# Kernel tuning notes

Measured on AMD Instinct MI355X. Metric: run time of the kernel, lower is better.

Reference implementation:

```python
import jax, jax.numpy as jnp
import numpy as np

S, N, DIN, DH, C, K, E = 12, 50000, 64, 128, 2, 3, 600000
HID = (DH + C) // 2  # 65
LN_EPS = 1e-5


def setup_inputs() -> dict:
    key = jax.random.key(0)
    ks = jax.random.split(key, 16)
    sc = 0.05
    inp = {
        'H': jax.random.normal(ks[0], (S, N, DIN), dtype=jnp.float32),
        'edge_index': jax.random.randint(ks[1], (2, E), 0, N, dtype=jnp.int64),
        # stacked gate params, gate order: 0=i, 1=f, 2=c(cell), 3=o
        'Wx': jax.random.normal(ks[2], (4, K, DIN, DH), dtype=jnp.float32) * sc,
        'bx': jnp.zeros((4, DH), dtype=jnp.float32),
        'Wh': jax.random.normal(ks[3], (4, K, DH, DH), dtype=jnp.float32) * sc,
        'bh': jnp.zeros((4, DH), dtype=jnp.float32),
        'b_gate': jnp.zeros((4, DH), dtype=jnp.float32),
        'wc': jax.random.normal(ks[4], (3, DH), dtype=jnp.float32) * sc,  # peephole: i, f, o
        'ln_gamma': jnp.ones((DH,), dtype=jnp.float32),
        'ln_beta': jnp.zeros((DH,), dtype=jnp.float32),
        'W1': jax.random.normal(ks[5], (DH, HID), dtype=jnp.float32) * sc,
        'b1': jnp.zeros((HID,), dtype=jnp.float32),
        'W2': jax.random.normal(ks[6], (HID, C), dtype=jnp.float32) * sc,
        'b2': jnp.zeros((C,), dtype=jnp.float32),
    }
    return inp


def _cheb_norm(edge_index):
    # sym-normalized, lambda_max=2 => scaled Laplacian Lhat = -D^-1/2 A D^-1/2 (zero diagonal)
    src, dst = edge_index[0], edge_index[1]
    ones = jnp.ones((src.shape[0],), dtype=jnp.float32)
    deg = jax.ops.segment_sum(ones, src, num_segments=N)
    dinv = jnp.where(deg > 0, jax.lax.rsqrt(jnp.maximum(deg, 1.0)), 0.0)
    norm = -dinv[src] * dinv[dst]
    return src, dst, norm


def _cheb_conv(x, W, b, src, dst, norm):
    # x: [N, Din]; W: [K, Din, Dout]. T0=x, T1=Lhat x, Tk=2 Lhat T_{k-1} - T_{k-2}
    Tx0 = x
    out = Tx0 @ W[0]
    if K > 1:
        Tx1 = jax.ops.segment_sum(norm[:, None] * Tx0[src], dst, num_segments=N)
        out = out + Tx1 @ W[1]
        for k in range(2, K):
            Tx2 = 2.0 * jax.ops.segment_sum(norm[:, None] * Tx1[src], dst, num_segments=N) - Tx0
            out = out + Tx2 @ W[k]
            Tx0, Tx1 = Tx1, Tx2
    return out + b


def _decoder(H, edge_index, Wx, bx, Wh, bh, b_gate, wc, ln_gamma, ln_beta, W1, b1, W2, b2):
    src, dst, norm = _cheb_norm(edge_index)

    def step(carry, x_t):
        h, c = carry
        gx = lambda g: _cheb_conv(x_t, Wx[g], bx[g], src, dst, norm)
        gh = lambda g: _cheb_conv(h, Wh[g], bh[g], src, dst, norm)
        i = jax.nn.sigmoid(gx(0) + gh(0) + wc[0] * c + b_gate[0])
        f = jax.nn.sigmoid(gx(1) + gh(1) + wc[1] * c + b_gate[1])
        t = jnp.tanh(gx(2) + gh(2) + b_gate[2])
        c = f * c + i * t
        o = jax.nn.sigmoid(gx(3) + gh(3) + wc[2] * c + b_gate[3])
        h = o * jnp.tanh(c)
        return (h, c), h

    h0 = jnp.zeros((N, DH), dtype=H.dtype)
    (_, _), X = jax.lax.scan(step, (h0, h0), H)  # X: [S, N, DH]

    X = jnp.tanh(X)
    # LayerNorm over conv_dim (last axis here)
    mu = jnp.mean(X, axis=-1, keepdims=True)
    var = jnp.mean(jnp.square(X - mu), axis=-1, keepdims=True)
    X = (X - mu) * jax.lax.rsqrt(var + LN_EPS) * ln_gamma + ln_beta
    # dropout in eval mode: identity
    X = jax.nn.relu(X @ W1 + b1) @ W2 + b2  # [S, N, C]
    X = jax.nn.sigmoid(X)
    return jnp.transpose(X, (1, 2, 0))  # [N, C, S]


def reference(H, edge_index, Wx, bx, Wh, bh, b_gate, wc, ln_gamma, ln_beta, W1, b1, W2, b2):
    return _decoder(H, edge_index, Wx, bx, Wh, bh, b_gate, wc, ln_gamma, ln_beta, W1, b1, W2, b2)
```

## Files before the change

### kernel.cpp

```cpp
#include <hip/hip_runtime.h>
#include <cstdint>
#include <cstddef>

#define S_DIM 12
#define N_NODE 50000
#define N_PAD 50048
#define N_P2 50176
#define D_IN 64
#define D_H 128
#define N_E 600000
#define K_TOT 576
#define N_COL 512
#define HID_P 80
#define N_HID 65
#define AXC 192

#define NB_PREP 1152
#define NB_DEG 2344
#define NB_SPMM 12500
#define NB_LN 782

typedef short bf16x8 __attribute__((ext_vector_type(8)));
typedef float f32x4 __attribute__((ext_vector_type(4)));

__device__ __forceinline__ float bf2f(unsigned short u){
  union { unsigned int i; float f; } v; v.i = ((unsigned int)u) << 16; return v.f;
}
__device__ __forceinline__ unsigned short f2bf(float f){
  union { float f; unsigned int i; } v; v.f = f;
  unsigned int x = v.i;
  return (unsigned short)((x + 0x7fffu + ((x >> 16) & 1u)) >> 16);
}
__device__ __forceinline__ float sigf(float x){ return 1.f/(1.f + __expf(-x)); }
__device__ __forceinline__ float ftanh(float x){
  x = fminf(fmaxf(x, -12.f), 12.f);
  float e = __expf(2.f*x);
  return (e - 1.f)/(e + 1.f);
}
__device__ __forceinline__ void gload16(const void* g, void* lds){
  __builtin_amdgcn_global_load_lds((const __attribute__((address_space(1))) unsigned int*)g,
                                   (__attribute__((address_space(3))) unsigned int*)lds, 16, 0, 0);
}
__device__ __forceinline__ void acc6(float* a, unsigned int p0, unsigned int p1, unsigned int p2, float w){
  unsigned int u[3] = {p0, p1, p2};
#pragma unroll
  for (int i=0;i<3;++i){
    a[2*i]   += w * bf2f((unsigned short)(u[i] & 0xffffu));
    a[2*i+1] += w * bf2f((unsigned short)(u[i] >> 16));
  }
}
__device__ __forceinline__ void acc8(float* a, uint4 h, float w){
  unsigned int u[4] = {h.x, h.y, h.z, h.w};
#pragma unroll
  for (int i=0;i<4;++i){
    a[2*i]   += w * bf2f((unsigned short)(u[i] & 0xffffu));
    a[2*i+1] += w * bf2f((unsigned short)(u[i] >> 16));
  }
}

__global__ void k_setup(const int* __restrict__ ei,
                        const float* __restrict__ Wx, const float* __restrict__ Wh,
                        const float* __restrict__ bx, const float* __restrict__ bh,
                        const float* __restrict__ bg, const float* __restrict__ W1,
                        const float* __restrict__ b1, const float* __restrict__ W2,
                        unsigned short* __restrict__ Bct, float* __restrict__ btot,
                        unsigned short* __restrict__ W1t, float* __restrict__ b1p,
                        float* __restrict__ W2p,
                        int* __restrict__ dsrc, int* __restrict__ ddst)
{
  int bb = blockIdx.x, tid = threadIdx.x;
  if (bb < NB_PREP){
    int idx = bb*256 + tid;
    if (idx < N_COL*K_TOT){
      int cc = idx / K_TOT, k = idx - cc*K_TOT;
      int g = (cc>>4)&3, d = (cc&15) + ((cc>>6)<<4);
      float v;
      if (k < 384){
        int kt = k >> 7, j = k & 127;
        const float* Wg = Wh + (size_t)g*3*128*128;
        if (kt == 0)      v = Wg[(size_t)j*128 + d] - Wg[(size_t)(256+j)*128 + d];
        else if (kt == 1) v = Wg[(size_t)(128+j)*128 + d];
        else              v = 2.f*Wg[(size_t)(256+j)*128 + d];
      } else {
        int kk = k - 384; int kt = kk >> 6, j = kk & 63;
        const float* Wg = Wx + (size_t)g*3*64*128;
        if (kt == 0)      v = Wg[(size_t)j*128 + d] - Wg[(size_t)(128+j)*128 + d];
        else if (kt == 1) v = Wg[(size_t)(64+j)*128 + d];
        else              v = 2.f*Wg[(size_t)(128+j)*128 + d];
      }
      Bct[(size_t)cc*K_TOT + k] = f2bf(v);
    }
    if (idx < N_COL) btot[idx] = bx[idx] + bh[idx] + bg[idx];
    if (idx < HID_P*D_H){ int c = idx >> 7, k = idx & 127;
      W1t[idx] = (c < N_HID) ? f2bf(W1[k*N_HID + c]) : (unsigned short)0; }
    if (idx < HID_P) b1p[idx] = (idx < N_HID) ? b1[idx] : 0.f;
    if (idx < HID_P*2){ int c = idx >> 1, j = idx & 1; W2p[idx] = (c < N_HID) ? W2[c*2 + j] : 0.f; }
  } else {
    int e = (bb - NB_PREP)*256 + tid;
    if (e < N_E){
      atomicAdd(&dsrc[ei[e]], 1);
      atomicAdd(&ddst[ei[N_E + e]], 1);
    }
  }
}

#define XP_STR 2056
__global__ __launch_bounds__(256,3) void k_xprep(const float* __restrict__ H,
                        unsigned short* __restrict__ Xtr, unsigned short* __restrict__ Axt)
{
  __shared__ unsigned short xls[12*XP_STR];
  int bb = blockIdx.x, tid = threadIdx.x;
  int n0 = bb*32;
  int nn = tid >> 3;
  int d  = (tid & 7)*8;
  int gn = n0 + nn;
#pragma unroll
  for (int t=0;t<12;++t){
    unsigned short u[8];
    if (gn < N_NODE){
      const float* hp = H + ((size_t)t*N_NODE + gn)*64 + d;
      float4 a = *(const float4*)hp;
      float4 b = *(const float4*)(hp+4);
      u[0]=f2bf(a.x); u[1]=f2bf(a.y); u[2]=f2bf(a.z); u[3]=f2bf(a.w);
      u[4]=f2bf(b.x); u[5]=f2bf(b.y); u[6]=f2bf(b.z); u[7]=f2bf(b.w);
    } else {
#pragma unroll
      for (int i=0;i<8;++i) u[i]=0;
    }
    *(int4*)(xls + t*XP_STR + nn*64 + d) = *(const int4*)u;
    *(int4*)(Axt + ((size_t)t*N_PAD + gn)*AXC + d) = *(const int4*)u;
    if (gn >= N_NODE){
      *(int4*)(Axt + ((size_t)t*N_PAD + gn)*AXC + 64 + d)  = *(const int4*)u;
      *(int4*)(Axt + ((size_t)t*N_PAD + gn)*AXC + 128 + d) = *(const int4*)u;
    }
  }
  __syncthreads();
#pragma unroll
  for (int rep=0; rep<8; ++rep){
    int cIdx = rep*256 + tid;
    int n = cIdx >> 6, dd = cIdx & 63;
    unsigned int w0[3], w1[3];
#pragma unroll
    for (int i=0;i<3;++i){
      unsigned short a0 = xls[(2*i  )*XP_STR + n*64 + dd];
      unsigned short a1 = xls[(2*i+1)*XP_STR + n*64 + dd];
      unsigned short b0 = xls[(6+2*i)*XP_STR + n*64 + dd];
      unsigned short b1 = xls[(7+2*i)*XP_STR + n*64 + dd];
      w0[i] = (unsigned int)a0 | ((unsigned int)a1<<16);
      w1[i] = (unsigned int)b0 | ((unsigned int)b1<<16);
    }
    size_t cell = ((size_t)(n0+n)*64 + dd)*6;
    unsigned int* p0 = (unsigned int*)(Xtr + cell);
    unsigned int* p1 = (unsigned int*)(Xtr + (size_t)N_PAD*384 + cell);
    p0[0]=w0[0]; p0[1]=w0[1]; p0[2]=w0[2];
    p1[0]=w1[0]; p1[1]=w1[1]; p1[2]=w1[2];
  }
}

__global__ void k_scan1d(const int* __restrict__ in, int* __restrict__ outp, int* __restrict__ part,
                         const int* __restrict__ dsrc, float* __restrict__ dinv){
  __shared__ int sm[256];
  int tid = threadIdx.x;
  int i = blockIdx.x*256 + tid;
  dinv[i] = (dsrc[i] > 0) ? rsqrtf((float)dsrc[i]) : 0.f;
  int v = in[i];
  int x = v;
  sm[tid] = x; __syncthreads();
  for (int off=1; off<256; off<<=1){
    int y = (tid >= off) ? sm[tid-off] : 0;
    __syncthreads();
    x += y; sm[tid] = x; __syncthreads();
  }
  outp[i] = x - v;
  if (tid == 255) part[blockIdx.x] = x;
}
__global__ void k_scan3f(const int* __restrict__ outp, const int* __restrict__ part,
                         int* __restrict__ offs){
  __shared__ int sm[256];
  int tid = threadIdx.x;
  int v = (tid < N_P2/256) ? part[tid] : 0;
  int x = v; sm[tid] = x; __syncthreads();
  for (int off=1; off<256; off<<=1){
    int y = (tid >= off) ? sm[tid-off] : 0;
    __syncthreads();
    x += y; sm[tid] = x; __syncthreads();
  }
  int pref = (blockIdx.x > 0) ? sm[blockIdx.x - 1] : 0;
  int i = blockIdx.x*256 + tid;
  offs[i] = outp[i] + pref;
}
__global__ void k_csr(const int* __restrict__ ei, const float* __restrict__ dinv,
                      const int* __restrict__ offs, int* __restrict__ cursor,
                      int2* __restrict__ cedge){
  int e = blockIdx.x*256 + threadIdx.x;
  if (e < N_E){
    int s = ei[e], d = ei[N_E + e];
    int pos = atomicAdd(&cursor[d], 1);
    float w = -dinv[s]*dinv[d];
    cedge[offs[d] + pos] = make_int2(s, __float_as_int(w));
  }
}

__global__ void k_xspmm1(const unsigned short* __restrict__ Xtr, unsigned short* __restrict__ Axt,
                         unsigned short* __restrict__ U1tr,
                         const int* __restrict__ offs, const int2* __restrict__ cedge){
  int bb = blockIdx.x;
  int h = (bb >= NB_SPMM) ? 1 : 0;
  const unsigned short* Xh = Xtr + (size_t)h*N_PAD*384;
  unsigned short* AxtH = Axt + (size_t)h*6*N_PAD*AXC;
  unsigned short* Uh = U1tr + (size_t)h*N_PAD*384;
  int n = (bb - h*NB_SPMM)*4 + (threadIdx.x >> 6);
  int l = threadIdx.x & 63;
  if (n >= N_NODE) return;
  int beg = offs[n], end = offs[n+1];
  int ce = end - 1;
  float a[6];
#pragma unroll
  for (int t=0;t<6;++t) a[t] = 0.f;
  for (int q = beg; q < end; q += 6){
    int2 e0 = cedge[min(q,   ce)];
    int2 e1 = cedge[min(q+1, ce)];
    int2 e2 = cedge[min(q+2, ce)];
    int2 e3 = cedge[min(q+3, ce)];
    int2 e4 = cedge[min(q+4, ce)];
    int2 e5 = cedge[min(q+5, ce)];
    float w0 = __int_as_float(e0.y);
    float w1 = (q+1 < end) ? __int_as_float(e1.y) : 0.f;
    float w2 = (q+2 < end) ? __int_as_float(e2.y) : 0.f;
    float w3 = (q+3 < end) ? __int_as_float(e3.y) : 0.f;
    float w4 = (q+4 < end) ? __int_as_float(e4.y) : 0.f;
    float w5 = (q+5 < end) ? __int_as_float(e5.y) : 0.f;
    const unsigned int* r0 = (const unsigned int*)(Xh + ((size_t)e0.x*64 + l)*6);
    const unsigned int* r1 = (const unsigned int*)(Xh + ((size_t)e1.x*64 + l)*6);
    const unsigned int* r2 = (const unsigned int*)(Xh + ((size_t)e2.x*64 + l)*6);
    const unsigned int* r3 = (const unsigned int*)(Xh + ((size_t)e3.x*64 + l)*6);
    const unsigned int* r4 = (const unsigned int*)(Xh + ((size_t)e4.x*64 + l)*6);
    const unsigned int* r5 = (const unsigned int*)(Xh + ((size_t)e5.x*64 + l)*6);
    unsigned int p00=r0[0], p01=r0[1], p02=r0[2];
    unsigned int p10=r1[0], p11=r1[1], p12=r1[2];
    unsigned int p20=r2[0], p21=r2[1], p22=r2[2];
    unsigned int p30=r3[0], p31=r3[1], p32=r3[2];
    unsigned int p40=r4[0], p41=r4[1], p42=r4[2];
    unsigned int p50=r5[0], p51=r5[1], p52=r5[2];
    acc6(a, p00, p01, p02, w0);
    acc6(a, p10, p11, p12, w1);
    acc6(a, p20, p21, p22, w2);
    acc6(a, p30, p31, p32, w3);
    acc6(a, p40, p41, p42, w4);
    acc6(a, p50, p51, p52, w5);
  }
  unsigned short u[6];
#pragma unroll
  for (int t=0;t<6;++t){
    u[t] = f2bf(a[t]);
    AxtH[((size_t)t*N_PAD + n)*AXC + 64 + l] = u[t];
  }
  unsigned int* op = (unsigned int*)(Uh + ((size_t)n*64 + l)*6);
#pragma unroll
  for (int i=0;i<3;++i) op[i] = (unsigned int)u[2*i] | ((unsigned int)u[2*i+1] << 16);
}
__global__ void k_xspmm2(const unsigned short* __restrict__ U1tr, unsigned short* __restrict__ Axt,
                         const int* __restrict__ offs, const int2* __restrict__ cedge){
  int bb = blockIdx.x;
  int h = (bb >= NB_SPMM) ? 1 : 0;
  const unsigned short* Uh = U1tr + (size_t)h*N_PAD*384;
  unsigned short* AxtH = Axt + (size_t)h*6*N_PAD*AXC;
  int n = (bb - h*NB_SPMM)*4 + (threadIdx.x >> 6);
  int l = threadIdx.x & 63;
  if (n >= N_NODE) return;
  int beg = offs[n], end = offs[n+1];
  int ce = end - 1;
  float a[6];
#pragma unroll
  for (int t=0;t<6;++t) a[t] = 0.f;
  for (int q = beg; q < end; q += 6){
    int2 e0 = cedge[min(q,   ce)];
    int2 e1 = cedge[min(q+1, ce)];
    int2 e2 = cedge[min(q+2, ce)];
    int2 e3 = cedge[min(q+3, ce)];
    int2 e4 = cedge[min(q+4, ce)];
    int2 e5 = cedge[min(q+5, ce)];
    float w0 = __int_as_float(e0.y);
    float w1 = (q+1 < end) ? __int_as_float(e1.y) : 0.f;
    float w2 = (q+2 < end) ? __int_as_float(e2.y) : 0.f;
    float w3 = (q+3 < end) ? __int_as_float(e3.y) : 0.f;
    float w4 = (q+4 < end) ? __int_as_float(e4.y) : 0.f;
    float w5 = (q+5 < end) ? __int_as_float(e5.y) : 0.f;
    const unsigned int* r0 = (const unsigned int*)(Uh + ((size_t)e0.x*64 + l)*6);
    const unsigned int* r1 = (const unsigned int*)(Uh + ((size_t)e1.x*64 + l)*6);
    const unsigned int* r2 = (const unsigned int*)(Uh + ((size_t)e2.x*64 + l)*6);
    const unsigned int* r3 = (const unsigned int*)(Uh + ((size_t)e3.x*64 + l)*6);
    const unsigned int* r4 = (const unsigned int*)(Uh + ((size_t)e4.x*64 + l)*6);
    const unsigned int* r5 = (const unsigned int*)(Uh + ((size_t)e5.x*64 + l)*6);
    unsigned int p00=r0[0], p01=r0[1], p02=r0[2];
    unsigned int p10=r1[0], p11=r1[1], p12=r1[2];
    unsigned int p20=r2[0], p21=r2[1], p22=r2[2];
    unsigned int p30=r3[0], p31=r3[1], p32=r3[2];
    unsigned int p40=r4[0], p41=r4[1], p42=r4[2];
    unsigned int p50=r5[0], p51=r5[1], p52=r5[2];
    acc6(a, p00, p01, p02, w0);
    acc6(a, p10, p11, p12, w1);
    acc6(a, p20, p21, p22, w2);
    acc6(a, p30, p31, p32, w3);
    acc6(a, p40, p41, p42, w4);
    acc6(a, p50, p51, p52, w5);
  }
#pragma unroll
  for (int t=0;t<6;++t)
    AxtH[((size_t)t*N_PAD + n)*AXC + 128 + l] = f2bf(a[t]);
}

__device__ __forceinline__ void spmm1_body(int n, int l,
    const unsigned short* __restrict__ Hc, unsigned short* __restrict__ U,
    const int* __restrict__ offs, const int2* __restrict__ cedge)
{
  if (n >= N_NODE) return;
  int sub = l >> 4, fl = l & 15;
  int beg = offs[n], end = offs[n+1];
  int ce = end - 1;
  float a[8];
#pragma unroll
  for (int j=0;j<8;++j) a[j] = 0.f;
  for (int q = beg; q < end; q += 16){
    int i0 = q + sub, i1 = q + 4 + sub, i2 = q + 8 + sub, i3 = q + 12 + sub;
    int2 e0 = cedge[min(i0, ce)];
    int2 e1 = cedge[min(i1, ce)];
    int2 e2 = cedge[min(i2, ce)];
    int2 e3 = cedge[min(i3, ce)];
    float w0 = (i0 < end) ? __int_as_float(e0.y) : 0.f;
    float w1 = (i1 < end) ? __int_as_float(e1.y) : 0.f;
    float w2 = (i2 < end) ? __int_as_float(e2.y) : 0.f;
    float w3 = (i3 < end) ? __int_as_float(e3.y) : 0.f;
    uint4 h0 = *(const uint4*)(Hc + (size_t)e0.x*128 + fl*8);
    uint4 h1 = *(const uint4*)(Hc + (size_t)e1.x*128 + fl*8);
    uint4 h2 = *(const uint4*)(Hc + (size_t)e2.x*128 + fl*8);
    uint4 h3 = *(const uint4*)(Hc + (size_t)e3.x*128 + fl*8);
    acc8(a, h0, w0);
    acc8(a, h1, w1);
    acc8(a, h2, w2);
    acc8(a, h3, w3);
  }
#pragma unroll
  for (int j=0;j<8;++j){
    a[j] += __shfl_xor(a[j], 16);
    a[j] += __shfl_xor(a[j], 32);
  }
  if (sub == 0){
    unsigned short o[8];
#pragma unroll
    for (int j=0;j<8;++j) o[j] = f2bf(a[j]);
    *(uint4*)(U + (size_t)n*256 + fl*8) = *(const uint4*)o;
  }
}

__global__ void k_spmm2(unsigned short* __restrict__ U,
                        const int* __restrict__ offs, const int2* __restrict__ cedge){
  int n = blockIdx.x*4 + (threadIdx.x >> 6);
  int l = threadIdx.x & 63;
  if (n >= N_NODE) return;
  int sub = l >> 4, fl = l & 15;
  int beg = offs[n], end = offs[n+1];
  int ce = end - 1;
  float a[8];
#pragma unroll
  for (int j=0;j<8;++j) a[j] = 0.f;
  for (int q = beg; q < end; q += 16){
    int i0 = q + sub, i1 = q + 4 + sub, i2 = q + 8 + sub, i3 = q + 12 + sub;
    int2 e0 = cedge[min(i0, ce)];
    int2 e1 = cedge[min(i1, ce)];
    int2 e2 = cedge[min(i2, ce)];
    int2 e3 = cedge[min(i3, ce)];
    float w0 = (i0 < end) ? __int_as_float(e0.y) : 0.f;
    float w1 = (i1 < end) ? __int_as_float(e1.y) : 0.f;
    float w2 = (i2 < end) ? __int_as_float(e2.y) : 0.f;
    float w3 = (i3 < end) ? __int_as_float(e3.y) : 0.f;
    uint4 h0 = *(const uint4*)(U + (size_t)e0.x*256 + fl*8);
    uint4 h1 = *(const uint4*)(U + (size_t)e1.x*256 + fl*8);
    uint4 h2 = *(const uint4*)(U + (size_t)e2.x*256 + fl*8);
    uint4 h3 = *(const uint4*)(U + (size_t)e3.x*256 + fl*8);
    acc8(a, h0, w0);
    acc8(a, h1, w1);
    acc8(a, h2, w2);
    acc8(a, h3, w3);
  }
#pragma unroll
  for (int j=0;j<8;++j){
    a[j] += __shfl_xor(a[j], 16);
    a[j] += __shfl_xor(a[j], 32);
  }
  if (sub == 0){
    unsigned short o[8];
#pragma unroll
    for (int j=0;j<8;++j) o[j] = f2bf(a[j]);
    *(uint4*)(U + (size_t)n*256 + 128 + fl*8) = *(const uint4*)o;
  }
}

__device__ __forceinline__ void lnmlp_body(int n0,
    const unsigned short* __restrict__ Hn,
    const unsigned short* __restrict__ W1t, const float* __restrict__ b1p,
    const float* __restrict__ W2p, const float* __restrict__ b2,
    const float* __restrict__ gam, const float* __restrict__ bet,
    float* __restrict__ out, int t)
{
  __shared__ __align__(16) unsigned short xn[64*128];
  __shared__ __align__(16) unsigned short w1s[HID_P*128];
  __shared__ float w2s[HID_P*2];
  __shared__ float b1s[HID_P];
  __shared__ float b2s[2];
  int tid = threadIdx.x;
  for (int i = tid; i < HID_P*128/8; i += 256) ((int4*)w1s)[i] = ((const int4*)W1t)[i];
  if (tid < HID_P*2) w2s[tid] = W2p[tid];
  if (tid < HID_P)   b1s[tid] = b1p[tid];
  if (tid < 2)       b2s[tid] = b2[tid];
  int row = tid >> 2, part = tid & 3;
  int n = n0 + row;
  float vals[32];
  float s = 0.f, ss = 0.f;
  if (n < N_NODE){
    const unsigned short* hp = Hn + (size_t)n*128 + part*32;
#pragma unroll
    for (int k=0;k<32;++k){
      float x = ftanh(bf2f(hp[k]));
      vals[k] = x; s += x; ss += x*x;
    }
  } else {
#pragma unroll
    for (int k=0;k<32;++k) vals[k] = 0.f;
  }
  s  += __shfl_xor(s,1);  s  += __shfl_xor(s,2);
  ss += __shfl_xor(ss,1); ss += __shfl_xor(ss,2);
  float mu = s * (1.f/128.f);
  float var = ss * (1.f/128.f) - mu*mu;
  float inv = rsqrtf(fmaxf(var, 0.f) + 1e-5f);
#pragma unroll
  for (int k=0;k<32;++k){
    int d = part*32 + k;
    xn[row*128 + d] = f2bf((vals[k]-mu)*inv*gam[d] + bet[d]);
  }
  __syncthreads();
  int w = tid >> 6, l = tid & 63;
  const f32x4 vzero = {0.f,0.f,0.f,0.f};
  f32x4 acc[5];
#pragma unroll
  for (int tj=0;tj<5;++tj) acc[tj] = vzero;
#pragma unroll
  for (int kk=0;kk<4;++kk){
    bf16x8 a = *(const bf16x8*)(xn + (w*16 + (l&15))*128 + kk*32 + (l>>4)*8);
#pragma unroll
    for (int tj=0;tj<5;++tj){
      bf16x8 b = *(const bf16x8*)(w1s + (tj*16 + (l&15))*128 + kk*32 + (l>>4)*8);
      acc[tj] = __builtin_amdgcn_mfma_f32_16x16x32_bf16(a, b, acc[tj], 0,0,0);
    }
  }
#pragma unroll
  for (int r=0;r<4;++r){
    int rn = n0 + w*16 + (l>>4)*4 + r;
    float p0 = 0.f, p1 = 0.f;
#pragma unroll
    for (int tj=0;tj<5;++tj){
      int col = tj*16 + (l&15);
      float hv = fmaxf(acc[tj][r] + b1s[col], 0.f);
      p0 += hv * w2s[col*2];
      p1 += hv * w2s[col*2+1];
    }
    p0 += __shfl_xor(p0,1); p0 += __shfl_xor(p0,2); p0 += __shfl_xor(p0,4); p0 += __shfl_xor(p0,8);
    p1 += __shfl_xor(p1,1); p1 += __shfl_xor(p1,2); p1 += __shfl_xor(p1,4); p1 += __shfl_xor(p1,8);
    if ((l & 15) == 0 && rn < N_NODE){
      float* op = out + (size_t)rn*24 + t;
      op[0]  = sigf(p0 + b2s[0]);
      op[12] = sigf(p1 + b2s[1]);
    }
  }
}

__global__ void k_sp1ln(const unsigned short* __restrict__ Hc, unsigned short* __restrict__ U,
                        const int* __restrict__ offs, const int2* __restrict__ cedge,
                        const unsigned short* __restrict__ W1t, const float* __restrict__ b1p,
                        const float* __restrict__ W2p, const float* __restrict__ b2,
                        const float* __restrict__ gam, const float* __restrict__ bet,
                        float* __restrict__ out, int tprev)
{
  int bb = blockIdx.x;
  if (bb < NB_LN){
    lnmlp_body(bb*64, Hc, W1t, b1p, W2p, b2, gam, bet, out, tprev);
  } else {
    spmm1_body((bb - NB_LN)*4 + (threadIdx.x >> 6), threadIdx.x & 63, Hc, U, offs, cedge);
  }
}

__global__ __launch_bounds__(256,2) void k_lnmlp(const unsigned short* __restrict__ Hn,
                        const unsigned short* __restrict__ W1t, const float* __restrict__ b1p,
                        const float* __restrict__ W2p, const float* __restrict__ b2,
                        const float* __restrict__ gam, const float* __restrict__ bet,
                        float* __restrict__ out, int t)
{
  lnmlp_body(blockIdx.x*64, Hn, W1t, b1p, W2p, b2, gam, bet, out, t);
}

__global__ __launch_bounds__(256,3) void k_gemm(
    const unsigned short* __restrict__ Hc, const unsigned short* __restrict__ U,
    const unsigned short* __restrict__ Axt,
    const unsigned short* __restrict__ Bct, const float* __restrict__ btot,
    const float* __restrict__ wc, unsigned short* __restrict__ cst,
    unsigned short* __restrict__ Hn, int it0)
{
  int L = blockIdx.y*4 + blockIdx.x;
  int xcd = L & 7, li = L >> 3;
  int by = xcd + ((li >> 2) << 3);
  int bx = li & 3;
  if (by >= N_PAD/128) return;
  __shared__ __align__(16) unsigned short As[128*64];
  __shared__ __align__(16) unsigned short Bs[128*64];
  int tid = threadIdx.x;
  int w = tid >> 6, l = tid & 63;
  int n0 = bx * 128;
  int m0 = by * 128;
  int wr = w >> 1, wn = w & 1;
  int dd = (((bx<<1) + wn) << 4) | (l & 15);
  float cof[4][4];
#pragma unroll
  for (int i=0;i<4;++i)
#pragma unroll
    for (int r=0;r<4;++r){
      int row = m0 + wr*64 + i*16 + (l>>4)*4 + r;
      cof[i][r] = bf2f(cst[(size_t)row*128 + dd]);
    }
  float b_i = btot[dd], b_f = btot[128+dd], b_t = btot[256+dd], b_o = btot[384+dd];
  float wci = wc[dd], wcf = wc[128+dd], wco = wc[256+dd];
  const f32x4 vzero = {0.f,0.f,0.f,0.f};
  f32x4 acc[4][4];
#pragma unroll
  for (int i=0;i<4;++i)
#pragma unroll
    for (int j=0;j<4;++j) acc[i][j] = vzero;
  for (int it=it0; it<9; ++it){
    const unsigned short* Ab; int astr, acol;
    if (it < 2)      { Ab = Hc;  astr = 128; acol = it*64; }
    else if (it < 6) { Ab = U;   astr = 256; acol = (it-2)*64; }
    else             { Ab = Axt; astr = AXC; acol = (it-6)*64; }
    if (it != it0) __syncthreads();
#pragma unroll
    for (int i=0;i<4;++i){
      int rr = w*32 + i*8;
      int row = rr + (l>>3);
      gload16(Ab  + (size_t)(m0+row)*astr + acol + (l&7)*8, (void*)(As + rr*64));
      gload16(Bct + (size_t)(n0+row)*K_TOT + it*64 + (l&7)*8, (void*)(Bs + rr*64));
    }
    __syncthreads();
#pragma unroll
    for (int kk=0; kk<2; ++kk){
      bf16x8 af[4], bfv[4];
#pragma unroll
      for (int i=0;i<4;++i) af[i]  = *(const bf16x8*)(As + (wr*64 + i*16 + (l&15))*64 + kk*32 + (l>>4)*8);
#pragma unroll
      for (int j=0;j<4;++j) bfv[j] = *(const bf16x8*)(Bs + (wn*64 + j*16 + (l&15))*64 + kk*32 + (l>>4)*8);
#pragma unroll
      for (int i=0;i<4;++i)
#pragma unroll
        for (int j=0;j<4;++j)
          acc[i][j] = __builtin_amdgcn_mfma_f32_16x16x32_bf16(af[i], bfv[j], acc[i][j], 0,0,0);
    }
  }
#pragma unroll
  for (int i=0;i<4;++i){
    int row0 = m0 + wr*64 + i*16 + (l>>4)*4;
#pragma unroll
    for (int r=0;r<4;++r){
      int row = row0 + r;
      float co = cof[i][r];
      float gi = sigf(acc[i][0][r] + b_i + wci*co);
      float gf = sigf(acc[i][1][r] + b_f + wcf*co);
      float tt = ftanh(acc[i][2][r] + b_t);
      float cn = gf*co + gi*tt;
      float go = sigf(acc[i][3][r] + b_o + wco*cn);
      float h = go * ftanh(cn);
      cst[(size_t)row*128 + dd] = f2bf(cn);
      Hn[(size_t)row*128 + dd] = f2bf(h);
    }
  }
}

extern "C" void kernel_launch(void* const* d_in, const int* in_sizes, int n_in,
                              void* d_out, int out_size, void* d_ws, size_t ws_size,
                              hipStream_t stream)
{
  const float* H   = (const float*)d_in[0];
  const int*   ei  = (const int*)d_in[1];
  const float* Wx  = (const float*)d_in[2];
  const float* bx  = (const float*)d_in[3];
  const float* Wh  = (const float*)d_in[4];
  const float* bh  = (const float*)d_in[5];
  const float* bg  = (const float*)d_in[6];
  const float* wc  = (const float*)d_in[7];
  const float* gam = (const float*)d_in[8];
  const float* bet = (const float*)d_in[9];
  const float* W1  = (const float*)d_in[10];
  const float* b1  = (const float*)d_in[11];
  const float* W2  = (const float*)d_in[12];
  const float* b2  = (const float*)d_in[13];
  float* out = (float*)d_out;
  (void)in_sizes; (void)n_in; (void)out_size; (void)ws_size;

  char* p = (char*)d_ws;
  auto alloc = [&](size_t bytes)->char*{ char* r = p; p += (bytes + 255) & ~(size_t)255; return r; };
  char* zbase = p;
  unsigned short* c_st = (unsigned short*)alloc((size_t)N_PAD*128*2);
  int* dsrc   = (int*)alloc((size_t)N_P2*4);
  int* ddst   = (int*)alloc((size_t)N_P2*4);
  int* cursor = (int*)alloc((size_t)N_P2*4);
  size_t zbytes = (size_t)(p - zbase);
  unsigned short* Hbuf0 = (unsigned short*)alloc((size_t)N_PAD*128*2);
  unsigned short* Hbuf1 = (unsigned short*)alloc((size_t)N_PAD*128*2);
  unsigned short* Ubuf  = (unsigned short*)alloc((size_t)N_PAD*256*2);
  unsigned short* Xtr   = (unsigned short*)alloc((size_t)N_PAD*768*2);
  unsigned short* U1tr  = (unsigned short*)alloc((size_t)N_PAD*768*2);
  unsigned short* Axt   = (unsigned short*)alloc((size_t)S_DIM*N_PAD*AXC*2);
  unsigned short* Bct   = (unsigned short*)alloc((size_t)N_COL*K_TOT*2);
  float*          btot  = (float*)alloc(N_COL*4);
  unsigned short* W1t   = (unsigned short*)alloc(HID_P*128*2);
  float*          b1p   = (float*)alloc(HID_P*4);
  float*          W2p   = (float*)alloc(HID_P*2*4);
  float*          dinv  = (float*)alloc((size_t)N_P2*4);
  int*            offs  = (int*)alloc((size_t)(N_P2+256)*4);
  int*            outp  = (int*)alloc((size_t)N_P2*4);
  int*            partb = (int*)alloc(256*4);
  int2*           cedge = (int2*)alloc((size_t)N_E*8);

  hipMemsetAsync(zbase, 0, zbytes, stream);
  k_setup<<<NB_PREP + NB_DEG, 256, 0, stream>>>(ei, Wx, Wh, bx, bh, bg,
      W1, b1, W2, Bct, btot, W1t, b1p, W2p, dsrc, ddst);
  k_xprep<<<N_PAD/32, 256, 0, stream>>>(H, Xtr, Axt);
  k_scan1d<<<N_P2/256, 256, 0, stream>>>(ddst, outp, partb, dsrc, dinv);
  k_scan3f<<<N_P2/256, 256, 0, stream>>>(outp, partb, offs);
  k_csr<<<NB_DEG, 256, 0, stream>>>(ei, dinv, offs, cursor, cedge);
  k_xspmm1<<<2*NB_SPMM, 256, 0, stream>>>(Xtr, Axt, U1tr, offs, cedge);
  k_xspmm2<<<2*NB_SPMM, 256, 0, stream>>>(U1tr, Axt, offs, cedge);

  k_gemm<<<dim3(4, 392), 256, 0, stream>>>(Hbuf0, Ubuf, Axt,
      Bct, btot, wc, c_st, Hbuf1, 6);
  for (int t = 1; t < S_DIM; ++t){
    unsigned short* Hc = (t & 1) ? Hbuf1 : Hbuf0;
    unsigned short* Hn = (t & 1) ? Hbuf0 : Hbuf1;
    k_sp1ln<<<NB_SPMM + NB_LN, 256, 0, stream>>>(Hc, Ubuf, offs, cedge,
        W1t, b1p, W2p, b2, gam, bet, out, t-1);
    k_spmm2<<<NB_SPMM, 256, 0, stream>>>(Ubuf, offs, cedge);
    k_gemm<<<dim3(4, 392), 256, 0, stream>>>(Hc, Ubuf,
        Axt + (size_t)t*N_PAD*AXC, Bct, btot, wc, c_st, Hn, 0);
  }
  k_lnmlp<<<NB_LN, 256, 0, stream>>>(Hbuf0, W1t, b1p, W2p, b2, gam, bet, out, 11);
}
```

Before: 1.905 ms.

## Split input-side Chebyshev SpMM and overlap most of it with timestep 1

Before the recurrence, only the input Chebyshev propagation columns needed for timesteps 0 and 1 are computed. The remaining input columns are computed as extra blocks folded into the timestep-1 spmm1/LN and spmm2 launches. This reorders k_sp1ln so spmm blocks come first, and in the GEMM it defers the cell-state and bias loads until after the MFMA loop to lower register pressure. The aim is to fill idle GPU capacity in the small recurrent kernels and shorten the serial prologue, at the cost of a larger, more divergent fused launch at t=1.

```diff
diff --git a/kernel.cpp b/kernel.cpp
--- a/kernel.cpp
+++ b/kernel.cpp
@@ -19,6 +19,7 @@
 #define NB_DEG 2344
 #define NB_SPMM 12500
 #define NB_LN 782
+#define NB_X 25000
 
 typedef short bf16x8 __attribute__((ext_vector_type(8)));
 typedef float f32x4 __attribute__((ext_vector_type(4)));
@@ -40,14 +41,6 @@
 __device__ __forceinline__ void gload16(const void* g, void* lds){
   __builtin_amdgcn_global_load_lds((const __attribute__((address_space(1))) unsigned int*)g,
                                    (__attribute__((address_space(3))) unsigned int*)lds, 16, 0, 0);
-}
-__device__ __forceinline__ void acc6(float* a, unsigned int p0, unsigned int p1, unsigned int p2, float w){
-  unsigned int u[3] = {p0, p1, p2};
-#pragma unroll
-  for (int i=0;i<3;++i){
-    a[2*i]   += w * bf2f((unsigned short)(u[i] & 0xffffu));
-    a[2*i+1] += w * bf2f((unsigned short)(u[i] >> 16));
-  }
 }
 __device__ __forceinline__ void acc8(float* a, uint4 h, float w){
   unsigned int u[4] = {h.x, h.y, h.z, h.w};
@@ -201,113 +194,102 @@
   }
 }
 
-__global__ void k_xspmm1(const unsigned short* __restrict__ Xtr, unsigned short* __restrict__ Axt,
-                         unsigned short* __restrict__ U1tr,
-                         const int* __restrict__ offs, const int2* __restrict__ cedge){
-  int bb = blockIdx.x;
-  int h = (bb >= NB_SPMM) ? 1 : 0;
-  const unsigned short* Xh = Xtr + (size_t)h*N_PAD*384;
-  unsigned short* AxtH = Axt + (size_t)h*6*N_PAD*AXC;
-  unsigned short* Uh = U1tr + (size_t)h*N_PAD*384;
-  int n = (bb - h*NB_SPMM)*4 + (threadIdx.x >> 6);
+template<int D0, int ND>
+__device__ __forceinline__ void xsp1_body(const unsigned short* __restrict__ Xh,
+    unsigned short* __restrict__ AxtH, unsigned short* __restrict__ Uh,
+    int n, int l, const int* __restrict__ offs, const int2* __restrict__ cedge)
+{
+  int beg = offs[n], end = offs[n+1];
+  int ce = end - 1;
+  float a[2*ND];
+#pragma unroll
+  for (int i=0;i<2*ND;++i) a[i] = 0.f;
+  for (int q = beg; q < end; q += 6){
+    int2 e[6]; float w[6];
+#pragma unroll
+    for (int j=0;j<6;++j){
+      e[j] = cedge[min(q+j, ce)];
+      w[j] = (q+j < end) ? __int_as_float(e[j].y) : 0.f;
+    }
+    unsigned int p[6][ND];
+#pragma unroll
+    for (int j=0;j<6;++j){
+      const unsigned int* r = (const unsigned int*)(Xh + ((size_t)e[j].x*64 + l)*6);
+#pragma unroll
+      for (int i=0;i<ND;++i) p[j][i] = r[D0+i];
+    }
+#pragma unroll
+    for (int j=0;j<6;++j)
+#pragma unroll
+      for (int i=0;i<ND;++i){
+        a[2*i]   += w[j]*bf2f((unsigned short)(p[j][i] & 0xffffu));
+        a[2*i+1] += w[j]*bf2f((unsigned short)(p[j][i] >> 16));
+      }
+  }
+  unsigned int* uc = (unsigned int*)(Uh + ((size_t)n*64 + l)*6);
+#pragma unroll
+  for (int i=0;i<ND;++i){
+    unsigned short u0 = f2bf(a[2*i]), u1 = f2bf(a[2*i+1]);
+    int tp = 2*(D0+i);
+    AxtH[((size_t)tp*N_PAD + n)*AXC + 64 + l]     = u0;
+    AxtH[((size_t)(tp+1)*N_PAD + n)*AXC + 64 + l] = u1;
+    uc[D0+i] = (unsigned int)u0 | ((unsigned int)u1 << 16);
+  }
+}
+template<int D0, int ND>
+__device__ __forceinline__ void xsp2_body(const unsigned short* __restrict__ Uh,
+    unsigned short* __restrict__ AxtH,
+    int n, int l, const int* __restrict__ offs, const int2* __restrict__ cedge)
+{
+  int beg = offs[n], end = offs[n+1];
+  int ce = end - 1;
+  float a[2*ND];
+#pragma unroll
+  for (int i=0;i<2*ND;++i) a[i] = 0.f;
+  for (int q = beg; q < end; q += 6){
+    int2 e[6]; float w[6];
+#pragma unroll
+    for (int j=0;j<6;++j){
+      e[j] = cedge[min(q+j, ce)];
+      w[j] = (q+j < end) ? __int_as_float(e[j].y) : 0.f;
+    }
+    unsigned int p[6][ND];
+#pragma unroll
+    for (int j=0;j<6;++j){
+      const unsigned int* r = (const unsigned int*)(Uh + ((size_t)e[j].x*64 + l)*6);
+#pragma unroll
+      for (int i=0;i<ND;++i) p[j][i] = r[D0+i];
+    }
+#pragma unroll
+    for (int j=0;j<6;++j)
+#pragma unroll
+      for (int i=0;i<ND;++i){
+        a[2*i]   += w[j]*bf2f((unsigned short)(p[j][i] & 0xffffu));
+        a[2*i+1] += w[j]*bf2f((unsigned short)(p[j][i] >> 16));
+      }
+  }
+#pragma unroll
+  for (int i=0;i<ND;++i){
+    int tp = 2*(D0+i);
+    AxtH[((size_t)tp*N_PAD + n)*AXC + 128 + l]     = f2bf(a[2*i]);
+    AxtH[((size_t)(tp+1)*N_PAD + n)*AXC + 128 + l] = f2bf(a[2*i+1]);
+  }
+}
+
+__global__ void k_xsp1_t01(const unsigned short* __restrict__ Xtr, unsigned short* __restrict__ Axt,
+                           unsigned short* __restrict__ U1tr,
+                           const int* __restrict__ offs, const int2* __restrict__ cedge){
+  int n = blockIdx.x*4 + (threadIdx.x >> 6);
   int l = threadIdx.x & 63;
   if (n >= N_NODE) return;
-  int beg = offs[n], end = offs[n+1];
-  int ce = end - 1;
-  float a[6];
-#pragma unroll
-  for (int t=0;t<6;++t) a[t] = 0.f;
-  for (int q = beg; q < end; q += 6){
-    int2 e0 = cedge[min(q,   ce)];
-    int2 e1 = cedge[min(q+1, ce)];
-    int2 e2 = cedge[min(q+2, ce)];
-    int2 e3 = cedge[min(q+3, ce)];
-    int2 e4 = cedge[min(q+4, ce)];
-    int2 e5 = cedge[min(q+5, ce)];
-    float w0 = __int_as_float(e0.y);
-    float w1 = (q+1 < end) ? __int_as_float(e1.y) : 0.f;
-    float w2 = (q+2 < end) ? __int_as_float(e2.y) : 0.f;
-    float w3 = (q+3 < end) ? __int_as_float(e3.y) : 0.f;
-    float w4 = (q+4 < end) ? __int_as_float(e4.y) : 0.f;
-    float w5 = (q+5 < end) ? __int_as_float(e5.y) : 0.f;
-    const unsigned int* r0 = (const unsigned int*)(Xh + ((size_t)e0.x*64 + l)*6);
-    const unsigned int* r1 = (const unsigned int*)(Xh + ((size_t)e1.x*64 + l)*6);
-    const unsigned int* r2 = (const unsigned int*)(Xh + ((size_t)e2.x*64 + l)*6);
-    const unsigned int* r3 = (const unsigned int*)(Xh + ((size_t)e3.x*64 + l)*6);
-    const unsigned int* r4 = (const unsigned int*)(Xh + ((size_t)e4.x*64 + l)*6);
-    const unsigned int* r5 = (const unsigned int*)(Xh + ((size_t)e5.x*64 + l)*6);
-    unsigned int p00=r0[0], p01=r0[1], p02=r0[2];
-    unsigned int p10=r1[0], p11=r1[1], p12=r1[2];
-    unsigned int p20=r2[0], p21=r2[1], p22=r2[2];
-    unsigned int p30=r3[0], p31=r3[1], p32=r3[2];
-    unsigned int p40=r4[0], p41=r4[1], p42=r4[2];
-    unsigned int p50=r5[0], p51=r5[1], p52=r5[2];
-    acc6(a, p00, p01, p02, w0);
-    acc6(a, p10, p11, p12, w1);
-    acc6(a, p20, p21, p22, w2);
-    acc6(a, p30, p31, p32, w3);
-    acc6(a, p40, p41, p42, w4);
-    acc6(a, p50, p51, p52, w5);
-  }
-  unsigned short u[6];
-#pragma unroll
-  for (int t=0;t<6;++t){
-    u[t] = f2bf(a[t]);
-    AxtH[((size_t)t*N_PAD + n)*AXC + 64 + l] = u[t];
-  }
-  unsigned int* op = (unsigned int*)(Uh + ((size_t)n*64 + l)*6);
-#pragma unroll
-  for (int i=0;i<3;++i) op[i] = (unsigned int)u[2*i] | ((unsigned int)u[2*i+1] << 16);
-}
-__global__ void k_xspmm2(const unsigned short* __restrict__ U1tr, unsigned short* __restrict__ Axt,
-                         const int* __restrict__ offs, const int2* __restrict__ cedge){
-  int bb = blockIdx.x;
-  int h = (bb >= NB_SPMM) ? 1 : 0;
-  const unsigned short* Uh = U1tr + (size_t)h*N_PAD*384;
-  unsigned short* AxtH = Axt + (size_t)h*6*N_PAD*AXC;
-  int n = (bb - h*NB_SPMM)*4 + (threadIdx.x >> 6);
+  xsp1_body<0,1>(Xtr, Axt, U1tr, n, l, offs, cedge);
+}
+__global__ void k_xsp2_t01(const unsigned short* __restrict__ U1tr, unsigned short* __restrict__ Axt,
+                           const int* __restrict__ offs, const int2* __restrict__ cedge){
+  int n = blockIdx.x*4 + (threadIdx.x >> 6);
   int l = threadIdx.x & 63;
   if (n >= N_NODE) return;
-  int beg = offs[n], end = offs[n+1];
-  int ce = end - 1;
-  float a[6];
-#pragma unroll
-  for (int t=0;t<6;++t) a[t] = 0.f;
-  for (int q = beg; q < end; q += 6){
-    int2 e0 = cedge[min(q,   ce)];
-    int2 e1 = cedge[min(q+1, ce)];
-    int2 e2 = cedge[min(q+2, ce)];
-    int2 e3 = cedge[min(q+3, ce)];
-    int2 e4 = cedge[min(q+4, ce)];
-    int2 e5 = cedge[min(q+5, ce)];
-    float w0 = __int_as_float(e0.y);
-    float w1 = (q+1 < end) ? __int_as_float(e1.y) : 0.f;
-    float w2 = (q+2 < end) ? __int_as_float(e2.y) : 0.f;
-    float w3 = (q+3 < end) ? __int_as_float(e3.y) : 0.f;
-    float w4 = (q+4 < end) ? __int_as_float(e4.y) : 0.f;
-    float w5 = (q+5 < end) ? __int_as_float(e5.y) : 0.f;
-    const unsigned int* r0 = (const unsigned int*)(Uh + ((size_t)e0.x*64 + l)*6);
-    const unsigned int* r1 = (const unsigned int*)(Uh + ((size_t)e1.x*64 + l)*6);
-    const unsigned int* r2 = (const unsigned int*)(Uh + ((size_t)e2.x*64 + l)*6);
-    const unsigned int* r3 = (const unsigned int*)(Uh + ((size_t)e3.x*64 + l)*6);
-    const unsigned int* r4 = (const unsigned int*)(Uh + ((size_t)e4.x*64 + l)*6);
-    const unsigned int* r5 = (const unsigned int*)(Uh + ((size_t)e5.x*64 + l)*6);
-    unsigned int p00=r0[0], p01=r0[1], p02=r0[2];
-    unsigned int p10=r1[0], p11=r1[1], p12=r1[2];
-    unsigned int p20=r2[0], p21=r2[1], p22=r2[2];
-    unsigned int p30=r3[0], p31=r3[1], p32=r3[2];
-    unsigned int p40=r4[0], p41=r4[1], p42=r4[2];
-    unsigned int p50=r5[0], p51=r5[1], p52=r5[2];
-    acc6(a, p00, p01, p02, w0);
-    acc6(a, p10, p11, p12, w1);
-    acc6(a, p20, p21, p22, w2);
-    acc6(a, p30, p31, p32, w3);
-    acc6(a, p40, p41, p42, w4);
-    acc6(a, p50, p51, p52, w5);
-  }
-#pragma unroll
-  for (int t=0;t<6;++t)
-    AxtH[((size_t)t*N_PAD + n)*AXC + 128 + l] = f2bf(a[t]);
+  xsp2_body<0,1>(U1tr, Axt, n, l, offs, cedge);
 }
 
 __device__ __forceinline__ void spmm1_body(int n, int l,
@@ -352,11 +334,10 @@
     *(uint4*)(U + (size_t)n*256 + fl*8) = *(const uint4*)o;
   }
 }
-
-__global__ void k_spmm2(unsigned short* __restrict__ U,
-                        const int* __restrict__ offs, const int2* __restrict__ cedge){
-  int n = blockIdx.x*4 + (threadIdx.x >> 6);
-  int l = threadIdx.x & 63;
+__device__ __forceinline__ void spmm2_body(int n, int l,
+    unsigned short* __restrict__ U,
+    const int* __restrict__ offs, const int2* __restrict__ cedge)
+{
   if (n >= N_NODE) return;
   int sub = l >> 4, fl = l & 15;
   int beg = offs[n], end = offs[n+1];
@@ -479,13 +460,52 @@
                         const unsigned short* __restrict__ W1t, const float* __restrict__ b1p,
                         const float* __restrict__ W2p, const float* __restrict__ b2,
                         const float* __restrict__ gam, const float* __restrict__ bet,
-                        float* __restrict__ out, int tprev)
+                        float* __restrict__ out, int tprev, int nx,
+                        const unsigned short* __restrict__ Xtr,
+                        unsigned short* __restrict__ Axt, unsigned short* __restrict__ U1tr)
 {
   int bb = blockIdx.x;
-  if (bb < NB_LN){
-    lnmlp_body(bb*64, Hc, W1t, b1p, W2p, b2, gam, bet, out, tprev);
+  int l = threadIdx.x & 63;
+  if (bb < NB_SPMM){
+    spmm1_body(bb*4 + (threadIdx.x >> 6), l, Hc, U, offs, cedge);
+  } else if (bb < NB_SPMM + nx){
+    int xb = bb - NB_SPMM;
+    if (xb < NB_SPMM){
+      int n = xb*4 + (threadIdx.x >> 6);
+      if (n < N_NODE)
+        xsp1_body<1,2>(Xtr, Axt, U1tr, n, l, offs, cedge);
+    } else {
+      int n = (xb - NB_SPMM)*4 + (threadIdx.x >> 6);
+      if (n < N_NODE)
+        xsp1_body<0,3>(Xtr + (size_t)N_PAD*384, Axt + (size_t)6*N_PAD*AXC,
+                       U1tr + (size_t)N_PAD*384, n, l, offs, cedge);
+    }
   } else {
-    spmm1_body((bb - NB_LN)*4 + (threadIdx.x >> 6), threadIdx.x & 63, Hc, U, offs, cedge);
+    lnmlp_body((bb - NB_SPMM - nx)*64, Hc, W1t, b1p, W2p, b2, gam, bet, out, tprev);
+  }
+}
+
+__global__ void k_spmm2(unsigned short* __restrict__ U,
+                        const int* __restrict__ offs, const int2* __restrict__ cedge,
+                        int nx, const unsigned short* __restrict__ U1tr,
+                        unsigned short* __restrict__ Axt)
+{
+  int bb = blockIdx.x;
+  int l = threadIdx.x & 63;
+  if (bb < NB_SPMM){
+    spmm2_body(bb*4 + (threadIdx.x >> 6), l, U, offs, cedge);
+  } else {
+    int xb = bb - NB_SPMM;
+    if (xb < NB_SPMM){
+      int n = xb*4 + (threadIdx.x >> 6);
+      if (n < N_NODE)
+        xsp2_body<1,2>(U1tr, Axt, n, l, offs, cedge);
+    } else {
+      int n = (xb - NB_SPMM)*4 + (threadIdx.x >> 6);
+      if (n < N_NODE)
+        xsp2_body<0,3>(U1tr + (size_t)N_PAD*384, Axt + (size_t)6*N_PAD*AXC,
+                       n, l, offs, cedge);
+    }
   }
 }
 
@@ -516,24 +536,13 @@
   int w = tid >> 6, l = tid & 63;
   int n0 = bx * 128;
   int m0 = by * 128;
-  int wr = w >> 1, wn = w & 1;
-  int dd = (((bx<<1) + wn) << 4) | (l & 15);
-  float cof[4][4];
-#pragma unroll
-  for (int i=0;i<4;++i)
-#pragma unroll
-    for (int r=0;r<4;++r){
-      int row = m0 + wr*64 + i*16 + (l>>4)*4 + r;
-      cof[i][r] = bf2f(cst[(size_t)row*128 + dd]);
-    }
-  float b_i = btot[dd], b_f = btot[128+dd], b_t = btot[256+dd], b_o = btot[384+dd];
-  float wci = wc[dd], wcf = wc[128+dd], wco = wc[256+dd];
   const f32x4 vzero = {0.f,0.f,0.f,0.f};
   f32x4 acc[4][4];
 #pragma unroll
   for (int i=0;i<4;++i)
 #pragma unroll
     for (int j=0;j<4;++j) acc[i][j] = vzero;
+  int wr = w >> 1, wn = w & 1;
   for (int it=it0; it<9; ++it){
     const unsigned short* Ab; int astr, acol;
     if (it < 2)      { Ab = Hc;  astr = 128; acol = it*64; }
@@ -562,13 +571,16 @@
           acc[i][j] = __builtin_amdgcn_mfma_f32_16x16x32_bf16(af[i], bfv[j], acc[i][j], 0,0,0);
     }
   }
+  int dd = (((bx<<1) + wn) << 4) | (l & 15);
+  float b_i = btot[dd], b_f = btot[128+dd], b_t = btot[256+dd], b_o = btot[384+dd];
+  float wci = wc[dd], wcf = wc[128+dd], wco = wc[256+dd];
 #pragma unroll
   for (int i=0;i<4;++i){
     int row0 = m0 + wr*64 + i*16 + (l>>4)*4;
 #pragma unroll
     for (int r=0;r<4;++r){
       int row = row0 + r;
-      float co = cof[i][r];
+      float co = bf2f(cst[(size_t)row*128 + dd]);
       float gi = sigf(acc[i][0][r] + b_i + wci*co);
       float gf = sigf(acc[i][1][r] + b_f + wcf*co);
       float tt = ftanh(acc[i][2][r] + b_t);
@@ -634,17 +646,18 @@
   k_scan1d<<<N_P2/256, 256, 0, stream>>>(ddst, outp, partb, dsrc, dinv);
   k_scan3f<<<N_P2/256, 256, 0, stream>>>(outp, partb, offs);
   k_csr<<<NB_DEG, 256, 0, stream>>>(ei, dinv, offs, cursor, cedge);
-  k_xspmm1<<<2*NB_SPMM, 256, 0, stream>>>(Xtr, Axt, U1tr, offs, cedge);
-  k_xspmm2<<<2*NB_SPMM, 256, 0, stream>>>(U1tr, Axt, offs, cedge);
+  k_xsp1_t01<<<NB_SPMM, 256, 0, stream>>>(Xtr, Axt, U1tr, offs, cedge);
+  k_xsp2_t01<<<NB_SPMM, 256, 0, stream>>>(U1tr, Axt, offs, cedge);
 
   k_gemm<<<dim3(4, 392), 256, 0, stream>>>(Hbuf0, Ubuf, Axt,
       Bct, btot, wc, c_st, Hbuf1, 6);
   for (int t = 1; t < S_DIM; ++t){
     unsigned short* Hc = (t & 1) ? Hbuf1 : Hbuf0;
     unsigned short* Hn = (t & 1) ? Hbuf0 : Hbuf1;
-    k_sp1ln<<<NB_SPMM + NB_LN, 256, 0, stream>>>(Hc, Ubuf, offs, cedge,
-        W1t, b1p, W2p, b2, gam, bet, out, t-1);
-    k_spmm2<<<NB_SPMM, 256, 0, stream>>>(Ubuf, offs, cedge);
+    int nx = (t == 1) ? NB_X : 0;
+    k_sp1ln<<<NB_SPMM + nx + NB_LN, 256, 0, stream>>>(Hc, Ubuf, offs, cedge,
+        W1t, b1p, W2p, b2, gam, bet, out, t-1, nx, Xtr, Axt, U1tr);
+    k_spmm2<<<NB_SPMM + nx, 256, 0, stream>>>(Ubuf, offs, cedge, nx, U1tr, Axt);
     k_gemm<<<dim3(4, 392), 256, 0, stream>>>(Hc, Ubuf,
         Axt + (size_t)t*N_PAD*AXC, Bct, btot, wc, c_st, Hn, 0);
   }
```

Result: slower. 1.990 ms (+4.4%).
